# Kernel optimization log

Measured on AMD Instinct MI355X. Metric: run time of the kernel, lower is better.

Reference implementation:

```python
import jax, jax.numpy as jnp
import numpy as np

NUM_EMBEDDINGS = 1024
EMBEDDING_DIM = 256


def setup_inputs() -> dict:
    key = jax.random.key(0)
    k1, k2 = jax.random.split(key)
    z = jax.random.normal(k1, (32, EMBEDDING_DIM, 32, 32), dtype=jnp.float32)
    codebook = jax.random.normal(k2, (NUM_EMBEDDINGS, EMBEDDING_DIM), dtype=jnp.float32)
    return {"z": z, "codebook": codebook}


def reference(z, codebook):
    # z: (B, C, H, W) -> (B, H, W, C) -> (B*H*W, C)
    B, C, H, W = z.shape
    z_bhwc = jnp.transpose(z, (0, 2, 3, 1))
    z_flat = z_bhwc.reshape(-1, C)  # (N, C)

    # pairwise squared distances: ||z||^2 + ||e||^2 - 2 z.e^T  -> (N, K)
    distances = (
        jnp.sum(z_flat ** 2, axis=1, keepdims=True)
        + jnp.sum(codebook ** 2, axis=1)
        - 2.0 * jnp.matmul(z_flat, codebook.T)
    )
    argmin_codewords = jnp.argmin(distances, axis=1)  # (N,)
    min_codewords = jax.nn.one_hot(argmin_codewords, NUM_EMBEDDINGS, dtype=jnp.float32)  # (N, K)

    # quantized latents via one-hot @ codebook, back to (B, C, H, W)
    z_quantized = jnp.matmul(min_codewords, codebook).reshape(B, H, W, C)
    z_quantized = jnp.transpose(z_quantized, (0, 3, 1, 2))
    return (min_codewords, z_quantized)
```

## Files before the change

### kernel.cpp

```cpp
#include <hip/hip_runtime.h>

#define N_ROWS 32768
#define K_CODES 1024
#define CDIM 256

typedef _Float16 half8 __attribute__((ext_vector_type(8)));
typedef _Float16 half4 __attribute__((ext_vector_type(4)));
typedef float floatx4 __attribute__((ext_vector_type(4)));

#define WS_ZH   0ull
#define WS_ZL   16777216ull
#define WS_CBH  33554432ull
#define WS_CBL  34078720ull
#define WS_CBN  34603008ull
#define WS_PART 34607104ull
#define WS_IDX  36704256ull
#define WS_NEED 36835328ull

__device__ __forceinline__ void g2lds16(const void* g, void* l) {
    __builtin_amdgcn_global_load_lds(
        (const __attribute__((address_space(1))) void*)g,
        (__attribute__((address_space(3))) void*)l, 16, 0, 0);
}


__global__ __launch_bounds__(64) void cb_prep(const float* __restrict__ cb,
                                              _Float16* __restrict__ cbh,
                                              _Float16* __restrict__ cbl,
                                              float* __restrict__ cbn) {
    int k = blockIdx.x;
    int lane = threadIdx.x;
    float4 v = reinterpret_cast<const float4*>(cb + k * CDIM)[lane];
    float s0 = v.x * 32.f, s1 = v.y * 32.f, s2 = v.z * 32.f, s3 = v.w * 32.f;
    half4 hv, lv;
    hv[0] = (_Float16)s0; lv[0] = (_Float16)(s0 - (float)hv[0]);
    hv[1] = (_Float16)s1; lv[1] = (_Float16)(s1 - (float)hv[1]);
    hv[2] = (_Float16)s2; lv[2] = (_Float16)(s2 - (float)hv[2]);
    hv[3] = (_Float16)s3; lv[3] = (_Float16)(s3 - (float)hv[3]);
    *reinterpret_cast<half4*>(&cbh[k * CDIM + lane * 4]) = hv;
    *reinterpret_cast<half4*>(&cbl[k * CDIM + lane * 4]) = lv;
    float s = s0 * s0 + s1 * s1 + s2 * s2 + s3 * s3;
    #pragma unroll
    for (int off = 32; off > 0; off >>= 1) s += __shfl_down(s, off);
    if (lane == 0) cbn[k] = s;
}

__global__ __launch_bounds__(256) void z_prep(const float* __restrict__ z,
                                              _Float16* __restrict__ zh,
                                              _Float16* __restrict__ zl) {
    __shared__ float t[64][68];
    int hwt = blockIdx.x & 15;
    int ct  = (blockIdx.x >> 4) & 3;
    int bb  = blockIdx.x >> 6;
    int tid = threadIdx.x;
    #pragma unroll
    for (int p = 0; p < 4; p++) {
        int e = p * 256 + tid;
        int c = e >> 4, h4 = e & 15;
        float4 v = *reinterpret_cast<const float4*>(
            &z[((bb * 256 + ct * 64 + c) << 10) + hwt * 64 + h4 * 4]);
        *reinterpret_cast<float4*>(&t[c][h4 * 4]) = v;
    }
    __syncthreads();
    #pragma unroll
    for (int p = 0; p < 4; p++) {
        int e = p * 256 + tid;
        int hw = e >> 4, c4 = e & 15;
        half4 hv, lv;
        #pragma unroll
        for (int j = 0; j < 4; j++) {
            float s = t[c4 * 4 + j][hw] * 32.f;
            _Float16 h = (_Float16)s;
            hv[j] = h;
            lv[j] = (_Float16)(s - (float)h);
        }
        size_t n = (size_t)(bb * 1024 + hwt * 64 + hw);
        *reinterpret_cast<half4*>(&zh[n * CDIM + ct * 64 + c4 * 4]) = hv;
        *reinterpret_cast<half4*>(&zl[n * CDIM + ct * 64 + c4 * 4]) = lv;
    }
}

__global__ __launch_bounds__(256) void vq_mfma(
    const _Float16* __restrict__ zh, const _Float16* __restrict__ zl,
    const _Float16* __restrict__ cbh, const _Float16* __restrict__ cbl,
    const float* __restrict__ cbn, unsigned long long* __restrict__ partial) {

    __shared__ _Float16 AhL[4096], AlL[4096], BhL[4096], BlL[4096];
    __shared__ float rvv[128][2];
    __shared__ int   rcc[128][2];

    const int tid = threadIdx.x;
    const int lane = tid & 63, wave = tid >> 6;
    const int wm = wave & 1, wn = wave >> 1;
    const int fm = lane & 15, fq = lane >> 4;
    const int codeTile = blockIdx.x & 7;
    const int rowTile  = blockIdx.x >> 3;
    const int rowBase = rowTile * 128, codeBase = codeTile * 128;

    floatx4 acc[16];
    #pragma unroll
    for (int i = 0; i < 16; i++) acc[i] = (floatx4)0.f;

    for (int kc = 0; kc < CDIM; kc += 32) {
        #pragma unroll
        for (int i = 0; i < 2; i++) {
            int G = i * 256 + tid;
            int q = G >> 7, r = G & 127;
            size_t ao = (size_t)(rowBase + r) * CDIM + kc + q * 8;
            size_t bo = (size_t)(codeBase + r) * CDIM + kc + q * 8;
            g2lds16(zh + ao,  &AhL[G * 8]);
            g2lds16(zl + ao,  &AlL[G * 8]);
            g2lds16(cbh + bo, &BhL[G * 8]);
            g2lds16(cbl + bo, &BlL[G * 8]);
        }
        __syncthreads();
        half8 ah[4], al[4], bh[4], bl[4];
        #pragma unroll
        for (int t = 0; t < 4; t++) {
            int ga = fq * 128 + wm * 64 + t * 16 + fm;
            int gb = fq * 128 + wn * 64 + t * 16 + fm;
            ah[t] = *reinterpret_cast<const half8*>(&AhL[ga * 8]);
            al[t] = *reinterpret_cast<const half8*>(&AlL[ga * 8]);
            bh[t] = *reinterpret_cast<const half8*>(&BhL[gb * 8]);
            bl[t] = *reinterpret_cast<const half8*>(&BlL[gb * 8]);
        }
        #pragma unroll
        for (int i = 0; i < 4; i++)
            #pragma unroll
            for (int j = 0; j < 4; j++) {
                acc[i*4+j] = __builtin_amdgcn_mfma_f32_16x16x32_f16(ah[i], bh[j], acc[i*4+j], 0, 0, 0);
                acc[i*4+j] = __builtin_amdgcn_mfma_f32_16x16x32_f16(al[i], bh[j], acc[i*4+j], 0, 0, 0);
                acc[i*4+j] = __builtin_amdgcn_mfma_f32_16x16x32_f16(ah[i], bl[j], acc[i*4+j], 0, 0, 0);
            }
        __syncthreads();
    }

    float cbnv[4];
    #pragma unroll
    for (int j = 0; j < 4; j++) cbnv[j] = cbn[codeBase + wn * 64 + j * 16 + fm];

    float bv[16]; int bc[16];
    #pragma unroll
    for (int i = 0; i < 4; i++)
        #pragma unroll
        for (int r = 0; r < 4; r++) {
            float best = 3.4e38f; int bcode = 0x7fffffff;
            #pragma unroll
            for (int j = 0; j < 4; j++) {
                float d = fmaf(-2.f, acc[i*4+j][r], cbnv[j]);
                int code = codeBase + wn * 64 + j * 16 + fm;
                if (d < best) { best = d; bcode = code; }
            }
            bv[i*4+r] = best; bc[i*4+r] = bcode;
        }
    #pragma unroll
    for (int s = 0; s < 16; s++) {
        float v = bv[s]; int c = bc[s];
        #pragma unroll
        for (int m = 1; m < 16; m <<= 1) {
            float ov = __shfl_xor(v, m, 64);
            int   oc = __shfl_xor(c, m, 64);
            if (ov < v || (ov == v && oc < c)) { v = ov; c = oc; }
        }
        bv[s] = v; bc[s] = c;
    }
    if (fm == 0) {
        #pragma unroll
        for (int i = 0; i < 4; i++)
            #pragma unroll
            for (int r = 0; r < 4; r++) {
                int row = wm * 64 + i * 16 + fq * 4 + r;
                rvv[row][wn] = bv[i*4+r];
                rcc[row][wn] = bc[i*4+r];
            }
    }
    __syncthreads();
    if (tid < 128) {
        float v0 = rvv[tid][0]; int c0 = rcc[tid][0];
        float v1 = rvv[tid][1]; int c1 = rcc[tid][1];
        if (v1 < v0 || (v1 == v0 && c1 < c0)) { v0 = v1; c0 = c1; }
        unsigned u = __float_as_uint(v0);
        u = (u & 0x80000000u) ? ~u : (u | 0x80000000u);
        partial[(size_t)(rowBase + tid) * 8 + codeTile] =
            ((unsigned long long)u << 32) | (unsigned)c0;
    }
}

__global__ __launch_bounds__(256) void vq_finalize(const unsigned long long* __restrict__ partial,
                                                   int* __restrict__ idx) {
    int row = blockIdx.x * 256 + threadIdx.x;
    unsigned long long best = partial[(size_t)row * 8];
    #pragma unroll
    for (int j = 1; j < 8; j++) {
        unsigned long long p = partial[(size_t)row * 8 + j];
        if (p < best) best = p;
    }
    idx[row] = (int)(best & 0xffffffffu);
}


__global__ __launch_bounds__(64) void cb_norms(const float* __restrict__ cb,
                                               float* __restrict__ cbn) {
    int k = blockIdx.x;
    int lane = threadIdx.x;
    float4 v = reinterpret_cast<const float4*>(cb + k * CDIM)[lane];
    float s = v.x * v.x + v.y * v.y + v.z * v.z + v.w * v.w;
    #pragma unroll
    for (int off = 32; off > 0; off >>= 1) s += __shfl_down(s, off);
    if (lane == 0) cbn[k] = s;
}

__global__ __launch_bounds__(256) void cb_transpose(const float* __restrict__ cb,
                                                    float* __restrict__ cbt) {
    __shared__ float t[32][33];
    int k0 = (blockIdx.x & 31) * 32;
    int c0 = (blockIdx.x >> 5) * 32;
    int lane = threadIdx.x & 31;
    int row = threadIdx.x >> 5;
    #pragma unroll
    for (int s = 0; s < 4; s++) {
        int r = row + s * 8;
        t[r][lane] = cb[(k0 + r) * CDIM + c0 + lane];
    }
    __syncthreads();
    #pragma unroll
    for (int s = 0; s < 4; s++) {
        int r = row + s * 8;
        cbt[(c0 + r) * K_CODES + k0 + lane] = t[lane][r];
    }
}

__global__ __launch_bounds__(512, 2) void vq_argmin(const float* __restrict__ z,
                                                    const float* __restrict__ cbt,
                                                    const float* __restrict__ cbn,
                                                    int* __restrict__ idx_out) {
    __shared__ float As[64][128];
    __shared__ float Bs[64][256];

    const int tid = threadIdx.x;
    const int tx = tid & 31;
    const int ty = tid >> 5;
    const int rowBase = blockIdx.x * 128;
    const int bb = rowBase >> 10;
    const int hwBase = rowBase & 1023;

    float minv[8];
    int   mini[8];
    #pragma unroll
    for (int i = 0; i < 8; i++) { minv[i] = 3.4e38f; mini[i] = 0; }

    for (int kt = 0; kt < K_CODES; kt += 256) {
        float acc[2][2][4][4];
        #pragma unroll
        for (int a = 0; a < 2; a++)
            #pragma unroll
            for (int b = 0; b < 2; b++)
                #pragma unroll
                for (int i = 0; i < 4; i++)
                    #pragma unroll
                    for (int j = 0; j < 4; j++) acc[a][b][i][j] = 0.f;

        for (int ccb = 0; ccb < CDIM; ccb += 64) {
            #pragma unroll
            for (int l = 0; l < 4; l++) {
                int f = tid + l * 512;
                int r4 = f & 31, c = f >> 5;
                float4 v = *reinterpret_cast<const float4*>(
                    &z[((bb * 256 + ccb + c) << 10) + hwBase + r4 * 4]);
                *reinterpret_cast<float4*>(&As[c][r4 * 4]) = v;
            }
            #pragma unroll
            for (int l = 0; l < 8; l++) {
                int f = tid + l * 512;
                int k4 = f & 63, c = f >> 6;
                float4 v = *reinterpret_cast<const float4*>(
                    &cbt[(ccb + c) * K_CODES + kt + k4 * 4]);
                *reinterpret_cast<float4*>(&Bs[c][k4 * 4]) = v;
            }
            __syncthreads();
            #pragma unroll 4
            for (int c = 0; c < 64; c++) {
                float4 a0 = *reinterpret_cast<const float4*>(&As[c][ty * 4]);
                float4 a1 = *reinterpret_cast<const float4*>(&As[c][64 + ty * 4]);
                float4 b0 = *reinterpret_cast<const float4*>(&Bs[c][tx * 4]);
                float4 b1 = *reinterpret_cast<const float4*>(&Bs[c][128 + tx * 4]);
                float av[2][4] = {{a0.x, a0.y, a0.z, a0.w}, {a1.x, a1.y, a1.z, a1.w}};
                float bw[2][4] = {{b0.x, b0.y, b0.z, b0.w}, {b1.x, b1.y, b1.z, b1.w}};
                #pragma unroll
                for (int ri = 0; ri < 2; ri++)
                    #pragma unroll
                    for (int i = 0; i < 4; i++)
                        #pragma unroll
                        for (int ci = 0; ci < 2; ci++)
                            #pragma unroll
                            for (int j = 0; j < 4; j++)
                                acc[ri][ci][i][j] =
                                    fmaf(av[ri][i], bw[ci][j], acc[ri][ci][i][j]);
            }
            __syncthreads();
        }
        #pragma unroll
        for (int ci = 0; ci < 2; ci++)
            #pragma unroll
            for (int j = 0; j < 4; j++) {
                int code = kt + ci * 128 + tx * 4 + j;
                float nrm = cbn[code];
                #pragma unroll
                for (int ri = 0; ri < 2; ri++)
                    #pragma unroll
                    for (int i = 0; i < 4; i++) {
                        float d = fmaf(-2.f, acc[ri][ci][i][j], nrm);
                        int r = ri * 4 + i;
                        if (d < minv[r]) { minv[r] = d; mini[r] = code; }
                    }
            }
    }

    __syncthreads();
    float (*rv)[32] = reinterpret_cast<float(*)[32]>(&As[0][0]);
    int   (*rix)[32] = reinterpret_cast<int(*)[32]>(&As[32][0]);
    #pragma unroll
    for (int ri = 0; ri < 2; ri++)
        #pragma unroll
        for (int i = 0; i < 4; i++) {
            int row = ri * 64 + ty * 4 + i;
            rv[row][tx] = minv[ri * 4 + i];
            rix[row][tx] = mini[ri * 4 + i];
        }
    __syncthreads();
    if (tid < 128) {
        float bvv = rv[tid][0]; int bii = rix[tid][0];
        #pragma unroll
        for (int t = 1; t < 32; t++) {
            float v = rv[tid][t]; int ii = rix[tid][t];
            if (v < bvv || (v == bvv && ii < bii)) { bvv = v; bii = ii; }
        }
        idx_out[rowBase + tid] = bii;
    }
}


__global__ __launch_bounds__(256) void onehot_fill(const int* __restrict__ idx,
                                                   float* __restrict__ out) {
    int i = blockIdx.x * 256 + threadIdx.x;
    int n  = i >> 8;
    int k4 = (i & 255) << 2;
    int id = idx[n];
    float4 v;
    v.x = (k4     == id) ? 1.f : 0.f;
    v.y = (k4 + 1 == id) ? 1.f : 0.f;
    v.z = (k4 + 2 == id) ? 1.f : 0.f;
    v.w = (k4 + 3 == id) ? 1.f : 0.f;
    reinterpret_cast<float4*>(out)[i] = v;
}

__global__ __launch_bounds__(256) void zq_fill(const int* __restrict__ idx,
                                               const float* __restrict__ cb,
                                               float* __restrict__ out) {
    int i  = blockIdx.x * 256 + threadIdx.x;
    int hw = i & 1023;
    int c  = (i >> 10) & 255;
    int b  = i >> 18;
    int n  = (b << 10) | hw;
    out[i] = cb[idx[n] * CDIM + c];
}

extern "C" void kernel_launch(void* const* d_in, const int* in_sizes, int n_in,
                              void* d_out, int out_size, void* d_ws, size_t ws_size,
                              hipStream_t stream) {
    const float* z  = (const float*)d_in[0];
    const float* cb = (const float*)d_in[1];
    float* out0 = (float*)d_out;
    float* out1 = out0 + (size_t)N_ROWS * K_CODES;

    if (ws_size >= WS_NEED) {
        _Float16* zh  = (_Float16*)((char*)d_ws + WS_ZH);
        _Float16* zl  = (_Float16*)((char*)d_ws + WS_ZL);
        _Float16* cbh = (_Float16*)((char*)d_ws + WS_CBH);
        _Float16* cbl = (_Float16*)((char*)d_ws + WS_CBL);
        float* cbn = (float*)((char*)d_ws + WS_CBN);
        unsigned long long* part = (unsigned long long*)((char*)d_ws + WS_PART);
        int* idx = (int*)((char*)d_ws + WS_IDX);

        cb_prep<<<K_CODES, 64, 0, stream>>>(cb, cbh, cbl, cbn);
        z_prep<<<2048, 256, 0, stream>>>(z, zh, zl);
        vq_mfma<<<2048, 256, 0, stream>>>(zh, zl, cbh, cbl, cbn, part);
        vq_finalize<<<N_ROWS / 256, 256, 0, stream>>>(part, idx);
        onehot_fill<<<(N_ROWS * K_CODES / 4) / 256, 256, 0, stream>>>(idx, out0);
        zq_fill<<<(N_ROWS * CDIM) / 256, 256, 0, stream>>>(idx, cb, out1);
    } else {
        float* cbn = (float*)d_ws;
        int*   idx = (int*)((char*)d_ws + 4096);
        float* cbt = (float*)((char*)d_ws + 4096 + 131072);

        cb_norms<<<K_CODES, 64, 0, stream>>>(cb, cbn);
        cb_transpose<<<256, 256, 0, stream>>>(cb, cbt);
        vq_argmin<<<N_ROWS / 128, 512, 0, stream>>>(z, cbt, cbn, idx);
        onehot_fill<<<(N_ROWS * K_CODES / 4) / 256, 256, 0, stream>>>(idx, out0);
        zq_fill<<<(N_ROWS * CDIM) / 256, 256, 0, stream>>>(idx, cb, out1);
    }
}
```

Measured before the change: 324.4 us.

## Switch VQ distance GEMM to 32x32 MFMA with chunked K-major layout and fuse finalize

Replaces the 16x16x32 MFMA tiles with 32x32x16 MFMA tiles, cutting the number of LDS fragment loads and shuffle-reduction stages per output. The z and codebook fp16 hi/lo buffers are stored in 32-element channel chunks, so each K-slice of a tile is one contiguous region for the global-to-LDS loads. The partial-argmin finalize kernel is merged into the one-hot writer, with one block per row, which removes a launch. Adds a launch-bounds occupancy hint, at the cost of larger accumulator vectors per wave.

```diff
diff --git a/kernel.cpp b/kernel.cpp
--- a/kernel.cpp
+++ b/kernel.cpp
@@ -6,7 +6,8 @@
 
 typedef _Float16 half8 __attribute__((ext_vector_type(8)));
 typedef _Float16 half4 __attribute__((ext_vector_type(4)));
-typedef float floatx4 __attribute__((ext_vector_type(4)));
+typedef float floatx16 __attribute__((ext_vector_type(16)));
+typedef unsigned long long ull;
 
 #define WS_ZH   0ull
 #define WS_ZL   16777216ull
@@ -37,11 +38,12 @@
     hv[1] = (_Float16)s1; lv[1] = (_Float16)(s1 - (float)hv[1]);
     hv[2] = (_Float16)s2; lv[2] = (_Float16)(s2 - (float)hv[2]);
     hv[3] = (_Float16)s3; lv[3] = (_Float16)(s3 - (float)hv[3]);
-    *reinterpret_cast<half4*>(&cbh[k * CDIM + lane * 4]) = hv;
-    *reinterpret_cast<half4*>(&cbl[k * CDIM + lane * 4]) = lv;
+    size_t off = (size_t)((lane >> 3) * K_CODES + k) * 32 + ((lane * 4) & 31);
+    *reinterpret_cast<half4*>(&cbh[off]) = hv;
+    *reinterpret_cast<half4*>(&cbl[off]) = lv;
     float s = s0 * s0 + s1 * s1 + s2 * s2 + s3 * s3;
     #pragma unroll
-    for (int off = 32; off > 0; off >>= 1) s += __shfl_down(s, off);
+    for (int off2 = 32; off2 > 0; off2 >>= 1) s += __shfl_down(s, off2);
     if (lane == 0) cbn[k] = s;
 }
 
@@ -74,16 +76,18 @@
             hv[j] = h;
             lv[j] = (_Float16)(s - (float)h);
         }
-        size_t n = (size_t)(bb * 1024 + hwt * 64 + hw);
-        *reinterpret_cast<half4*>(&zh[n * CDIM + ct * 64 + c4 * 4]) = hv;
-        *reinterpret_cast<half4*>(&zl[n * CDIM + ct * 64 + c4 * 4]) = lv;
-    }
-}
-
-__global__ __launch_bounds__(256) void vq_mfma(
+        int n = bb * 1024 + hwt * 64 + hw;
+        int cg = ct * 64 + c4 * 4;
+        size_t off = (size_t)((cg >> 5) * N_ROWS + n) * 32 + (cg & 31);
+        *reinterpret_cast<half4*>(&zh[off]) = hv;
+        *reinterpret_cast<half4*>(&zl[off]) = lv;
+    }
+}
+
+__global__ __launch_bounds__(256, 3) void vq_mfma32(
     const _Float16* __restrict__ zh, const _Float16* __restrict__ zl,
     const _Float16* __restrict__ cbh, const _Float16* __restrict__ cbl,
-    const float* __restrict__ cbn, unsigned long long* __restrict__ partial) {
+    const float* __restrict__ cbn, ull* __restrict__ partial) {
 
     __shared__ _Float16 AhL[4096], AlL[4096], BhL[4096], BlL[4096];
     __shared__ float rvv[128][2];
@@ -92,88 +96,85 @@
     const int tid = threadIdx.x;
     const int lane = tid & 63, wave = tid >> 6;
     const int wm = wave & 1, wn = wave >> 1;
-    const int fm = lane & 15, fq = lane >> 4;
+    const int fm = lane & 31, fq = lane >> 5;
     const int codeTile = blockIdx.x & 7;
     const int rowTile  = blockIdx.x >> 3;
     const int rowBase = rowTile * 128, codeBase = codeTile * 128;
 
-    floatx4 acc[16];
-    #pragma unroll
-    for (int i = 0; i < 16; i++) acc[i] = (floatx4)0.f;
+    floatx16 acc[4];
+    #pragma unroll
+    for (int i = 0; i < 4; i++) acc[i] = (floatx16)0.f;
 
     for (int kc = 0; kc < CDIM; kc += 32) {
+        const int cc = kc >> 5;
+        const size_t ab = (size_t)(cc * N_ROWS + rowBase) * 32;
+        const size_t bb = (size_t)(cc * K_CODES + codeBase) * 32;
         #pragma unroll
         for (int i = 0; i < 2; i++) {
             int G = i * 256 + tid;
             int q = G >> 7, r = G & 127;
-            size_t ao = (size_t)(rowBase + r) * CDIM + kc + q * 8;
-            size_t bo = (size_t)(codeBase + r) * CDIM + kc + q * 8;
-            g2lds16(zh + ao,  &AhL[G * 8]);
-            g2lds16(zl + ao,  &AlL[G * 8]);
-            g2lds16(cbh + bo, &BhL[G * 8]);
-            g2lds16(cbl + bo, &BlL[G * 8]);
+            size_t so = (size_t)r * 32 + q * 8;
+            g2lds16(zh + ab + so,  &AhL[G * 8]);
+            g2lds16(zl + ab + so,  &AlL[G * 8]);
+            g2lds16(cbh + bb + so, &BhL[G * 8]);
+            g2lds16(cbl + bb + so, &BlL[G * 8]);
         }
         __syncthreads();
-        half8 ah[4], al[4], bh[4], bl[4];
-        #pragma unroll
-        for (int t = 0; t < 4; t++) {
-            int ga = fq * 128 + wm * 64 + t * 16 + fm;
-            int gb = fq * 128 + wn * 64 + t * 16 + fm;
-            ah[t] = *reinterpret_cast<const half8*>(&AhL[ga * 8]);
-            al[t] = *reinterpret_cast<const half8*>(&AlL[ga * 8]);
-            bh[t] = *reinterpret_cast<const half8*>(&BhL[gb * 8]);
-            bl[t] = *reinterpret_cast<const half8*>(&BlL[gb * 8]);
-        }
-        #pragma unroll
-        for (int i = 0; i < 4; i++)
-            #pragma unroll
-            for (int j = 0; j < 4; j++) {
-                acc[i*4+j] = __builtin_amdgcn_mfma_f32_16x16x32_f16(ah[i], bh[j], acc[i*4+j], 0, 0, 0);
-                acc[i*4+j] = __builtin_amdgcn_mfma_f32_16x16x32_f16(al[i], bh[j], acc[i*4+j], 0, 0, 0);
-                acc[i*4+j] = __builtin_amdgcn_mfma_f32_16x16x32_f16(ah[i], bl[j], acc[i*4+j], 0, 0, 0);
-            }
+        #pragma unroll
+        for (int s = 0; s < 2; s++) {
+            int q = s * 2 + fq;
+            half8 ah[2], al[2], bh[2], bl[2];
+            #pragma unroll
+            for (int i = 0; i < 2; i++) {
+                int ga = q * 128 + wm * 64 + i * 32 + fm;
+                ah[i] = *reinterpret_cast<const half8*>(&AhL[ga * 8]);
+                al[i] = *reinterpret_cast<const half8*>(&AlL[ga * 8]);
+            }
+            #pragma unroll
+            for (int j = 0; j < 2; j++) {
+                int gb = q * 128 + wn * 64 + j * 32 + fm;
+                bh[j] = *reinterpret_cast<const half8*>(&BhL[gb * 8]);
+                bl[j] = *reinterpret_cast<const half8*>(&BlL[gb * 8]);
+            }
+            #pragma unroll
+            for (int i = 0; i < 2; i++)
+                #pragma unroll
+                for (int j = 0; j < 2; j++) {
+                    acc[i*2+j] = __builtin_amdgcn_mfma_f32_32x32x16_f16(ah[i], bh[j], acc[i*2+j], 0, 0, 0);
+                    acc[i*2+j] = __builtin_amdgcn_mfma_f32_32x32x16_f16(al[i], bh[j], acc[i*2+j], 0, 0, 0);
+                    acc[i*2+j] = __builtin_amdgcn_mfma_f32_32x32x16_f16(ah[i], bl[j], acc[i*2+j], 0, 0, 0);
+                }
+        }
         __syncthreads();
     }
 
-    float cbnv[4];
-    #pragma unroll
-    for (int j = 0; j < 4; j++) cbnv[j] = cbn[codeBase + wn * 64 + j * 16 + fm];
-
-    float bv[16]; int bc[16];
-    #pragma unroll
-    for (int i = 0; i < 4; i++)
-        #pragma unroll
-        for (int r = 0; r < 4; r++) {
+    float cbnv[2];
+    #pragma unroll
+    for (int j = 0; j < 2; j++) cbnv[j] = cbn[codeBase + wn * 64 + j * 32 + fm];
+
+    #pragma unroll
+    for (int i = 0; i < 2; i++)
+        #pragma unroll
+        for (int r = 0; r < 16; r++) {
             float best = 3.4e38f; int bcode = 0x7fffffff;
             #pragma unroll
-            for (int j = 0; j < 4; j++) {
-                float d = fmaf(-2.f, acc[i*4+j][r], cbnv[j]);
-                int code = codeBase + wn * 64 + j * 16 + fm;
+            for (int j = 0; j < 2; j++) {
+                float d = fmaf(-2.f, acc[i*2+j][r], cbnv[j]);
+                int code = codeBase + wn * 64 + j * 32 + fm;
                 if (d < best) { best = d; bcode = code; }
             }
-            bv[i*4+r] = best; bc[i*4+r] = bcode;
-        }
-    #pragma unroll
-    for (int s = 0; s < 16; s++) {
-        float v = bv[s]; int c = bc[s];
-        #pragma unroll
-        for (int m = 1; m < 16; m <<= 1) {
-            float ov = __shfl_xor(v, m, 64);
-            int   oc = __shfl_xor(c, m, 64);
-            if (ov < v || (ov == v && oc < c)) { v = ov; c = oc; }
-        }
-        bv[s] = v; bc[s] = c;
-    }
-    if (fm == 0) {
-        #pragma unroll
-        for (int i = 0; i < 4; i++)
-            #pragma unroll
-            for (int r = 0; r < 4; r++) {
-                int row = wm * 64 + i * 16 + fq * 4 + r;
-                rvv[row][wn] = bv[i*4+r];
-                rcc[row][wn] = bc[i*4+r];
-            }
-    }
+            #pragma unroll
+            for (int m = 1; m < 32; m <<= 1) {
+                float ov = __shfl_xor(best, m, 64);
+                int   oc = __shfl_xor(bcode, m, 64);
+                if (ov < best || (ov == best && oc < bcode)) { best = ov; bcode = oc; }
+            }
+            if (fm == 0) {
+                int row = wm * 64 + i * 32 + (r & 3) + 8 * (r >> 2) + 4 * fq;
+                rvv[row][wn] = best;
+                rcc[row][wn] = bcode;
+            }
+        }
     __syncthreads();
     if (tid < 128) {
         float v0 = rvv[tid][0]; int c0 = rcc[tid][0];
@@ -182,20 +183,49 @@
         unsigned u = __float_as_uint(v0);
         u = (u & 0x80000000u) ? ~u : (u | 0x80000000u);
         partial[(size_t)(rowBase + tid) * 8 + codeTile] =
-            ((unsigned long long)u << 32) | (unsigned)c0;
-    }
-}
-
-__global__ __launch_bounds__(256) void vq_finalize(const unsigned long long* __restrict__ partial,
-                                                   int* __restrict__ idx) {
-    int row = blockIdx.x * 256 + threadIdx.x;
-    unsigned long long best = partial[(size_t)row * 8];
-    #pragma unroll
-    for (int j = 1; j < 8; j++) {
-        unsigned long long p = partial[(size_t)row * 8 + j];
-        if (p < best) best = p;
-    }
-    idx[row] = (int)(best & 0xffffffffu);
+            ((ull)u << 32) | (unsigned)c0;
+    }
+}
+
+__global__ __launch_bounds__(256) void onehot_fin(const ull* __restrict__ partial,
+                                                  int* __restrict__ idx,
+                                                  float* __restrict__ out) {
+    int row = blockIdx.x;
+    __shared__ int sid;
+    if (threadIdx.x < 64) {
+        ull v = (threadIdx.x < 8) ? partial[(size_t)row * 8 + threadIdx.x]
+                                  : ~0ull;
+        #pragma unroll
+        for (int m = 1; m < 8; m <<= 1) {
+            ull o = __shfl_xor(v, m, 64);
+            if (o < v) v = o;
+        }
+        if (threadIdx.x == 0) {
+            int id = (int)(v & 0xffffffffu);
+            sid = id;
+            idx[row] = id;
+        }
+    }
+    __syncthreads();
+    int id = sid;
+    int k4 = threadIdx.x << 2;
+    float4 v4;
+    v4.x = (k4     == id) ? 1.f : 0.f;
+    v4.y = (k4 + 1 == id) ? 1.f : 0.f;
+    v4.z = (k4 + 2 == id) ? 1.f : 0.f;
+    v4.w = (k4 + 3 == id) ? 1.f : 0.f;
+    reinterpret_cast<float4*>(out)[(size_t)row * 256 + threadIdx.x] = v4;
+}
+
+__global__ __launch_bounds__(256) void zq_fill(const int* __restrict__ idx,
+                                               const float* __restrict__ cb,
+                                               float* __restrict__ out) {
+    int i  = blockIdx.x * 256 + threadIdx.x;
+    int hw = i & 1023;
+    int c  = (i >> 10) & 255;
+    int b  = i >> 18;
+    int n  = (b << 10) | hw;
+    out[i] = cb[idx[n] * CDIM + c];
 }
 
 
@@ -339,7 +369,6 @@
     }
 }
 
-
 __global__ __launch_bounds__(256) void onehot_fill(const int* __restrict__ idx,
                                                    float* __restrict__ out) {
     int i = blockIdx.x * 256 + threadIdx.x;
@@ -354,17 +383,6 @@
     reinterpret_cast<float4*>(out)[i] = v;
 }
 
-__global__ __launch_bounds__(256) void zq_fill(const int* __restrict__ idx,
-                                               const float* __restrict__ cb,
-                                               float* __restrict__ out) {
-    int i  = blockIdx.x * 256 + threadIdx.x;
-    int hw = i & 1023;
-    int c  = (i >> 10) & 255;
-    int b  = i >> 18;
-    int n  = (b << 10) | hw;
-    out[i] = cb[idx[n] * CDIM + c];
-}
-
 extern "C" void kernel_launch(void* const* d_in, const int* in_sizes, int n_in,
                               void* d_out, int out_size, void* d_ws, size_t ws_size,
                               hipStream_t stream) {
@@ -379,14 +397,13 @@
         _Float16* cbh = (_Float16*)((char*)d_ws + WS_CBH);
         _Float16* cbl = (_Float16*)((char*)d_ws + WS_CBL);
         float* cbn = (float*)((char*)d_ws + WS_CBN);
-        unsigned long long* part = (unsigned long long*)((char*)d_ws + WS_PART);
+        ull* part = (ull*)((char*)d_ws + WS_PART);
         int* idx = (int*)((char*)d_ws + WS_IDX);
 
         cb_prep<<<K_CODES, 64, 0, stream>>>(cb, cbh, cbl, cbn);
         z_prep<<<2048, 256, 0, stream>>>(z, zh, zl);
-        vq_mfma<<<2048, 256, 0, stream>>>(zh, zl, cbh, cbl, cbn, part);
-        vq_finalize<<<N_ROWS / 256, 256, 0, stream>>>(part, idx);
-        onehot_fill<<<(N_ROWS * K_CODES / 4) / 256, 256, 0, stream>>>(idx, out0);
+        vq_mfma32<<<2048, 256, 0, stream>>>(zh, zl, cbh, cbl, cbn, part);
+        onehot_fin<<<N_ROWS, 256, 0, stream>>>(part, idx, out0);
         zq_fill<<<(N_ROWS * CDIM) / 256, 256, 0, stream>>>(idx, cb, out1);
     } else {
         float* cbn = (float*)d_ws;
```

New measurement: 297.6 us. -8.3%, faster.
